# Kernel tuning notes

Hardware: AMD Instinct MI355X
Metric: run time of the kernel (lower is better)

Reference implementation:

```python
import jax, jax.numpy as jnp
import numpy as np

T, OBS, MLP, H, ACT = 2048, 512, 1024, 1024, 16
SIG0 = 0.5  # config['noise_std'] -> NoisyLinear init_std


def mish(x):
    return x * jnp.tanh(jax.nn.softplus(x))


def noisy_linear(x, wm, ws, bm, bs, kw, kb):
    # NoisyLinear: perturbed weights/bias sampled per forward call from the key.
    # In the original, the same key is tiled across the vmapped time axis, so a
    # single noise sample is shared by all timesteps -> one sample here.
    w = wm + ws * jax.random.normal(kw, wm.shape, wm.dtype)
    b = bm + bs * jax.random.normal(kb, bm.shape, bm.dtype)
    return x @ w.T + b


def setup_inputs() -> dict:
    key = jax.random.key(0)
    ks = jax.random.split(key, 8)

    def lin(k, o, i):
        lim = 1.0 / np.sqrt(i)
        return jax.random.uniform(k, (o, i), jnp.float32, -lim, lim)

    return {
        "x": jax.random.normal(ks[0], (T, OBS), jnp.float32),
        "state": jnp.zeros((H,), jnp.float32),
        "start": jax.random.randint(ks[1], (T,), 0, 2, dtype=jnp.int32),
        "done": jnp.zeros((T,), jnp.int32),
        "pre_wm": lin(ks[2], MLP, OBS),
        "pre_ws": jnp.full((MLP, OBS), SIG0, jnp.float32),
        "pre_bm": jnp.zeros((MLP,), jnp.float32),
        "pre_bs": jnp.full((MLP,), SIG0, jnp.float32),
        "gru_wih": lin(ks[3], 3 * H, MLP),
        "gru_whh": lin(ks[4], 3 * H, H),
        "gru_b": jnp.zeros((3 * H,), jnp.float32),
        "gru_bn": jnp.zeros((H,), jnp.float32),
        "p1_wm": lin(ks[5], MLP, H),
        "p1_ws": jnp.full((MLP, H), SIG0, jnp.float32),
        "p1_bm": jnp.zeros((MLP,), jnp.float32),
        "p1_bs": jnp.full((MLP,), SIG0, jnp.float32),
        "p2_wm": lin(ks[6], MLP, MLP),
        "p2_ws": jnp.full((MLP, MLP), SIG0, jnp.float32),
        "p2_bm": jnp.zeros((MLP,), jnp.float32),
        "p2_bs": jnp.full((MLP,), SIG0, jnp.float32),
        "p3_wm": lin(ks[7], ACT, MLP) * 0.01,  # final_layer_init: small last layer
        "p3_ws": jnp.full((ACT, MLP), SIG0, jnp.float32),
        "p3_bm": jnp.zeros((ACT,), jnp.float32),
        "p3_bs": jnp.full((ACT,), SIG0, jnp.float32),
    }


def _forward(x, state, start, pre_wm, pre_ws, pre_bm, pre_bs, gru_wih, gru_whh,
             gru_b, gru_bn, p1_wm, p1_ws, p1_bm, p1_bs, p2_wm, p2_ws, p2_bm,
             p2_bs, p3_wm, p3_ws, p3_bm, p3_bs):
    nk = jax.random.split(jax.random.key(7), 8)
    # pre MLP: NoisyLinear + mish, vectorized over time
    z = mish(noisy_linear(x, pre_wm, pre_ws, pre_bm, pre_bs, nk[0], nk[1]))  # [T, MLP]
    # input-side GRU gates precomputed as one big GEMM (equinox GRUCell math)
    igates = z @ gru_wih.T + gru_b  # [T, 3H]
    keep = (1 - start).astype(z.dtype)  # [T]; 0 where an episode starts -> reset h

    def step(h, inp):
        ig, k = inp
        h_in = h * k  # state * logical_not(start)
        hg = h_in @ gru_whh.T  # [3H]
        ir, iz, in_ = jnp.split(ig, 3)
        hr, hz, hn = jnp.split(hg, 3)
        r = jax.nn.sigmoid(ir + hr)
        u = jax.nn.sigmoid(iz + hz)
        n = jnp.tanh(in_ + r * (hn + gru_bn))
        h_new = n + u * (h_in - n)  # == (1-u)*n + u*h_in
        return h_new, h_new

    final_state, states = jax.lax.scan(step, state, (igates, keep))  # states: [T, H]
    # post MLP: NoisyLinear+mish, NoisyLinear+mish, NoisyLinear (final)
    y = mish(noisy_linear(states, p1_wm, p1_ws, p1_bm, p1_bs, nk[2], nk[3]))
    y = mish(noisy_linear(y, p2_wm, p2_ws, p2_bm, p2_bs, nk[4], nk[5]))
    y = noisy_linear(y, p3_wm, p3_ws, p3_bm, p3_bs, nk[6], nk[7])  # [T, ACT]
    return y, final_state


def reference(x, state, start, done, pre_wm, pre_ws, pre_bm, pre_bs, gru_wih,
              gru_whh, gru_b, gru_bn, p1_wm, p1_ws, p1_bm, p1_bs, p2_wm, p2_ws,
              p2_bm, p2_bs, p3_wm, p3_ws, p3_bm, p3_bs):
    del done  # threaded through the scan in the original but never used
    return _forward(x, state, start, pre_wm, pre_ws, pre_bm, pre_bs, gru_wih,
                    gru_whh, gru_b, gru_bn, p1_wm, p1_ws, p1_bm, p1_bs, p2_wm,
                    p2_ws, p2_bm, p2_bs, p3_wm, p3_ws, p3_bm, p3_bs)
```

## Files before the change

kernel.cpp:

```cpp
#include <hip/hip_runtime.h>
#include <cstdint>
#include <cstddef>

#define T_ 2048
#define OBS_ 512
#define MLP_ 1024
#define H_ 1024
#define ACT_ 16
#define H3_ 3072
#define NROUNDS 20

typedef short bf16x8 __attribute__((ext_vector_type(8)));
typedef float f32x4 __attribute__((ext_vector_type(4)));

__host__ __device__ __forceinline__ uint32_t rotl32(uint32_t v, int d) {
  return (v << d) | (v >> (32 - d));
}
__host__ __device__ __forceinline__ void tf2x32(uint32_t k0, uint32_t k1,
                                                uint32_t x0, uint32_t x1,
                                                uint32_t& o0, uint32_t& o1) {
  uint32_t ks2 = k0 ^ k1 ^ 0x1BD11BDAu;
  x0 += k0; x1 += k1;
  x0 += x1; x1 = rotl32(x1, 13); x1 ^= x0;
  x0 += x1; x1 = rotl32(x1, 15); x1 ^= x0;
  x0 += x1; x1 = rotl32(x1, 26); x1 ^= x0;
  x0 += x1; x1 = rotl32(x1, 6);  x1 ^= x0;
  x0 += k1; x1 += ks2 + 1u;
  x0 += x1; x1 = rotl32(x1, 17); x1 ^= x0;
  x0 += x1; x1 = rotl32(x1, 29); x1 ^= x0;
  x0 += x1; x1 = rotl32(x1, 16); x1 ^= x0;
  x0 += x1; x1 = rotl32(x1, 24); x1 ^= x0;
  x0 += ks2; x1 += k0 + 2u;
  x0 += x1; x1 = rotl32(x1, 13); x1 ^= x0;
  x0 += x1; x1 = rotl32(x1, 15); x1 ^= x0;
  x0 += x1; x1 = rotl32(x1, 26); x1 ^= x0;
  x0 += x1; x1 = rotl32(x1, 6);  x1 ^= x0;
  x0 += k0; x1 += k1 + 3u;
  x0 += x1; x1 = rotl32(x1, 17); x1 ^= x0;
  x0 += x1; x1 = rotl32(x1, 29); x1 ^= x0;
  x0 += x1; x1 = rotl32(x1, 16); x1 ^= x0;
  x0 += x1; x1 = rotl32(x1, 24); x1 ^= x0;
  x0 += k1; x1 += ks2 + 4u;
  x0 += x1; x1 = rotl32(x1, 13); x1 ^= x0;
  x0 += x1; x1 = rotl32(x1, 15); x1 ^= x0;
  x0 += x1; x1 = rotl32(x1, 26); x1 ^= x0;
  x0 += x1; x1 = rotl32(x1, 6);  x1 ^= x0;
  x0 += ks2; x1 += k0 + 5u;
  o0 = x0; o1 = x1;
}

__device__ __forceinline__ float erfinv_f32(float x) {
  float w = -log1pf(-x * x);
  float p;
  if (w < 5.0f) {
    w = w - 2.5f;
    p = 2.81022636e-08f;
    p = fmaf(p, w, 3.43273939e-07f);
    p = fmaf(p, w, -3.5233877e-06f);
    p = fmaf(p, w, -4.39150654e-06f);
    p = fmaf(p, w, 0.00021858087f);
    p = fmaf(p, w, -0.00125372503f);
    p = fmaf(p, w, -0.00417768164f);
    p = fmaf(p, w, 0.246640727f);
    p = fmaf(p, w, 1.50140941f);
  } else {
    w = sqrtf(w) - 3.0f;
    p = -0.000200214257f;
    p = fmaf(p, w, 0.000100950558f);
    p = fmaf(p, w, 0.00134934322f);
    p = fmaf(p, w, -0.00367342844f);
    p = fmaf(p, w, 0.00573950773f);
    p = fmaf(p, w, -0.0076224613f);
    p = fmaf(p, w, 0.00943887047f);
    p = fmaf(p, w, 1.00167406f);
    p = fmaf(p, w, 2.83297682f);
  }
  return p * x;
}

__device__ __forceinline__ float bits_to_normal(uint32_t bits) {
  const float lo = -0.99999994f;
  float f = __uint_as_float((bits >> 9) | 0x3f800000u) - 1.0f;
  float u = fmaf(f, 2.0f, lo);
  u = fmaxf(lo, u);
  return 1.41421356237f * erfinv_f32(u);
}

__device__ __forceinline__ float sigmoidf_(float x) {
  return 1.0f / (1.0f + expf(-x));
}
__device__ __forceinline__ float mishf_(float x) {
  float sp = fmaxf(x, 0.0f) + log1pf(expf(-fabsf(x)));
  return x * tanhf(sp);
}

__device__ __forceinline__ ushort f2bf(float v) {
  uint32_t u = __float_as_uint(v);
  uint32_t r = (u + 0x7FFFu + ((u >> 16) & 1u)) >> 16;
  return (ushort)r;
}
__device__ __forceinline__ float bf2f(ushort b) {
  return __uint_as_float(((uint32_t)b) << 16);
}

struct NoiseDesc {
  const float* wm; const float* ws;
  ushort* dh; ushort* dl; float* df;
  uint32_t k0, k1, base, mode;
};
struct NoiseArgs { NoiseDesc d[8]; uint32_t total; int* meta_zero; };

__global__ __launch_bounds__(256) void k_gen_noise(NoiseArgs a) {
  if (blockIdx.x < 16) a.meta_zero[blockIdx.x * 256 + threadIdx.x] = 0;
  uint32_t idx = blockIdx.x * 256u + threadIdx.x;
  for (; idx < a.total; idx += gridDim.x * 256u) {
    int ti = 0;
#pragma unroll
    for (int i = 1; i < 8; ++i) if (idx >= a.d[i].base) ti = i;
    NoiseDesc dd = a.d[ti];
    uint32_t j = idx - dd.base;
    uint32_t b1, b2;
    tf2x32(dd.k0, dd.k1, 0u, j, b1, b2);
    float v = fmaf(dd.ws[j], bits_to_normal(b1 ^ b2), dd.wm[j]);
    if (dd.mode) {
      ushort hb = f2bf(v);
      dd.dh[j] = hb;
      dd.dl[j] = f2bf(v - bf2f(hb));
    } else {
      dd.df[j] = v;
    }
  }
}

__global__ __launch_bounds__(256) void k_split(const float* __restrict__ in,
                                               ushort* __restrict__ h,
                                               ushort* __restrict__ l, int n4) {
  int i = blockIdx.x * 256 + threadIdx.x;
  if (i >= n4) return;
  float4 v = ((const float4*)in)[i];
  ushort4 hb, lb;
  hb.x = f2bf(v.x); lb.x = f2bf(v.x - bf2f(hb.x));
  hb.y = f2bf(v.y); lb.y = f2bf(v.y - bf2f(hb.y));
  hb.z = f2bf(v.z); lb.z = f2bf(v.z - bf2f(hb.z));
  hb.w = f2bf(v.w); lb.w = f2bf(v.w - bf2f(hb.w));
  ((ushort4*)h)[i] = hb;
  ((ushort4*)l)[i] = lb;
}

template <int ACTF, int OUTM>
__global__ __launch_bounds__(256, 2) void k_mgemm(
    const ushort* __restrict__ Ah, const ushort* __restrict__ Al,
    const ushort* __restrict__ Wh, const ushort* __restrict__ Wl,
    const float* __restrict__ bias,
    float* __restrict__ Cf, ushort* __restrict__ Ch, ushort* __restrict__ Cl,
    int K, int Nreal, int ldc) {
  __shared__ ushort sA[2][128 * 32];
  __shared__ ushort sW[2][128 * 32];
  const int tid = threadIdx.x;
  const int m0 = blockIdx.y * 128, n0 = blockIdx.x * 128;
  const int wid = tid >> 6, lane = tid & 63;
  const int wm = (wid >> 1) * 64, wn = (wid & 1) * 64;
  const int lr = lane & 15, lk = lane >> 4;
  const int r0 = tid >> 2;
  const int c0 = (tid & 3) * 8;
  f32x4 acc[4][4] = {};
  for (int k0 = 0; k0 < K; k0 += 32) {
    const size_t aoff0 = (size_t)(m0 + r0) * K + k0 + c0;
    const size_t aoff1 = (size_t)(m0 + r0 + 64) * K + k0 + c0;
    const size_t woff0 = (size_t)(n0 + r0) * K + k0 + c0;
    const size_t woff1 = (size_t)(n0 + r0 + 64) * K + k0 + c0;
    int4 ah0 = *(const int4*)(Ah + aoff0);
    int4 ah1 = *(const int4*)(Ah + aoff1);
    int4 al0 = *(const int4*)(Al + aoff0);
    int4 al1 = *(const int4*)(Al + aoff1);
    int4 wh0 = *(const int4*)(Wh + woff0);
    int4 wh1 = *(const int4*)(Wh + woff1);
    int4 wl0 = *(const int4*)(Wl + woff0);
    int4 wl1 = *(const int4*)(Wl + woff1);
    __syncthreads();
    *(int4*)(&sA[0][r0 * 32 + c0]) = ah0;
    *(int4*)(&sA[0][(r0 + 64) * 32 + c0]) = ah1;
    *(int4*)(&sA[1][r0 * 32 + c0]) = al0;
    *(int4*)(&sA[1][(r0 + 64) * 32 + c0]) = al1;
    *(int4*)(&sW[0][r0 * 32 + c0]) = wh0;
    *(int4*)(&sW[0][(r0 + 64) * 32 + c0]) = wh1;
    *(int4*)(&sW[1][r0 * 32 + c0]) = wl0;
    *(int4*)(&sW[1][(r0 + 64) * 32 + c0]) = wl1;
    __syncthreads();
    bf16x8 fah[4], fal[4], fwh[4], fwl[4];
#pragma unroll
    for (int f = 0; f < 4; ++f) {
      int ar = (wm + f * 16 + lr) * 32 + lk * 8;
      fah[f] = *(const bf16x8*)(&sA[0][ar]);
      fal[f] = *(const bf16x8*)(&sA[1][ar]);
      int wr = (wn + f * 16 + lr) * 32 + lk * 8;
      fwh[f] = *(const bf16x8*)(&sW[0][wr]);
      fwl[f] = *(const bf16x8*)(&sW[1][wr]);
    }
#pragma unroll
    for (int mf = 0; mf < 4; ++mf)
#pragma unroll
      for (int nf = 0; nf < 4; ++nf) {
        acc[mf][nf] = __builtin_amdgcn_mfma_f32_16x16x32_bf16(fah[mf], fwh[nf], acc[mf][nf], 0, 0, 0);
        acc[mf][nf] = __builtin_amdgcn_mfma_f32_16x16x32_bf16(fah[mf], fwl[nf], acc[mf][nf], 0, 0, 0);
        acc[mf][nf] = __builtin_amdgcn_mfma_f32_16x16x32_bf16(fal[mf], fwh[nf], acc[mf][nf], 0, 0, 0);
      }
  }
#pragma unroll
  for (int mf = 0; mf < 4; ++mf)
#pragma unroll
    for (int nf = 0; nf < 4; ++nf) {
      int col = n0 + wn + nf * 16 + lr;
      if (col >= Nreal) continue;
      float bv = bias[col];
#pragma unroll
      for (int r = 0; r < 4; ++r) {
        int row = m0 + wm + mf * 16 + lk * 4 + r;
        float v = acc[mf][nf][r] + bv;
        if (ACTF) v = mishf_(v);
        if (OUTM == 0) {
          Cf[(size_t)row * ldc + col] = v;
        } else {
          ushort hb = f2bf(v);
          Ch[(size_t)row * ldc + col] = hb;
          Cl[(size_t)row * ldc + col] = f2bf(v - bf2f(hb));
        }
      }
    }
}

__global__ void k_li(const int* __restrict__ start, int* __restrict__ li,
                     int* __restrict__ counts) {
  int t = blockIdx.x * 256 + threadIdx.x;
  if (t >= T_) return;
  int l = 0, tt = t;
  while (tt > 0 && start[tt] == 0) { tt--; l++; }
  li[t] = l;
  if (t > 0) atomicAdd(&counts[l], 1);
}

__global__ __launch_bounds__(256) void k_offsets(const int* __restrict__ counts,
                                                 int* __restrict__ offsets) {
  __shared__ int a[2048], b[2048];
  int tid = threadIdx.x;
  for (int i = tid; i < 2048; i += 256) a[i] = counts[i];
  __syncthreads();
  int* cur = a; int* nxt = b;
  for (int d = 1; d < 2048; d <<= 1) {
    for (int i = tid; i < 2048; i += 256)
      nxt[i] = cur[i] + (i >= d ? cur[i - d] : 0);
    __syncthreads();
    int* t_ = cur; cur = nxt; nxt = t_;
  }
  for (int i = tid; i < 2048; i += 256)
    offsets[i] = (i == 0) ? 0 : cur[i - 1];
}

__global__ void k_scatter(const int* __restrict__ li, const int* __restrict__ offsets,
                          int* __restrict__ cursors, int* __restrict__ list) {
  int t = blockIdx.x * 256 + threadIdx.x;
  if (t <= 0 || t >= T_) return;
  int l = li[t];
  int pos = atomicAdd(&cursors[l], 1);
  list[offsets[l] + pos] = t;
}

__global__ __launch_bounds__(256) void k_hg0(
    const float* __restrict__ whhf, const float* __restrict__ state0,
    const int* __restrict__ start, float* __restrict__ hg0) {
  const float keep0 = 1.0f - (float)start[0];
  int gw = blockIdx.x * 4 + (threadIdx.x >> 6);
  int lane = threadIdx.x & 63;
  for (int r = gw * 3; r < gw * 3 + 3 && r < H3_; ++r) {
    const float* wr = whhf + (size_t)r * H_;
    float s = 0.f;
    for (int c = lane; c < H_; c += 64) s = fmaf(wr[c], state0[c] * keep0, s);
    for (int o = 32; o; o >>= 1) s += __shfl_down(s, o, 64);
    if (lane == 0) hg0[r] = s;
  }
}

__global__ __launch_bounds__(256) void k_gate0(
    const float* __restrict__ ig, const float* __restrict__ gbn,
    const float* __restrict__ state0, const int* __restrict__ start,
    const int* __restrict__ counts, const int* __restrict__ offsets,
    const int* __restrict__ list, const float* __restrict__ hg0,
    ushort* __restrict__ st_h, ushort* __restrict__ st_l) {
  const float keep0 = 1.0f - (float)start[0];
  int cnt0 = counts[0], off0 = offsets[0];
  int total = (cnt0 + 1) * H_;
  for (int e = blockIdx.x * 256 + threadIdx.x; e < total; e += gridDim.x * 256) {
    int s = e >> 10, i = e & (H_ - 1);
    int t; float hin, hr, hz, hn;
    if (s == 0) {
      t = 0; hin = state0[i] * keep0;
      hr = hg0[i]; hz = hg0[H_ + i]; hn = hg0[2 * H_ + i];
    } else {
      t = list[off0 + s - 1]; hin = 0.f; hr = 0.f; hz = 0.f; hn = 0.f;
    }
    float ir = ig[(size_t)t * H3_ + i];
    float iz = ig[(size_t)t * H3_ + H_ + i];
    float in_ = ig[(size_t)t * H3_ + 2 * H_ + i];
    float r = sigmoidf_(ir + hr), u = sigmoidf_(iz + hz);
    float n = tanhf(in_ + r * (hn + gbn[i]));
    float v = n + u * (hin - n);
    ushort hb = f2bf(v);
    st_h[(size_t)t * H_ + i] = hb;
    st_l[(size_t)t * H_ + i] = f2bf(v - bf2f(hb));
  }
}

struct SMemRound {
  ushort Hs[2][64][40];
  ushort Bs[2][96][40];
  int tl[64];
};

__global__ __launch_bounds__(256) void k_round(
    const int k, const float* __restrict__ ig,
    const ushort* __restrict__ whh_h, const ushort* __restrict__ whh_l,
    const float* __restrict__ gbn,
    const int* __restrict__ counts, const int* __restrict__ offsets,
    const int* __restrict__ list,
    ushort* __restrict__ st_h, ushort* __restrict__ st_l) {
  const int cnt = counts[k];
  if (cnt == 0) return;
  __shared__ SMemRound sm;
  const int tid = threadIdx.x, bid = blockIdx.x, nb = gridDim.x;
  const int off = offsets[k];
  const int mtiles = (cnt + 63) >> 6;
  const int tiles = mtiles << 5;

  const int wid = tid >> 6, lane = tid & 63;
  const int lr = lane & 15, lk = lane >> 4;
  const int wm = (wid >> 1) * 32;
  const int wi = wid & 1;

  const int a_koct = tid & 3, a_row = (tid >> 2) & 63;
  int blev[3], brow[3], bkoct[3];
#pragma unroll
  for (int j = 0; j < 3; ++j) {
    int c = tid + 256 * j;
    blev[j] = c / 384;
    int rem = c - blev[j] * 384;
    brow[j] = rem >> 2;
    bkoct[j] = rem & 3;
  }
  const ushort* bsp[3];
#pragma unroll
  for (int j = 0; j < 3; ++j) bsp[j] = blev[j] ? whh_l : whh_h;

  for (int tile = bid; tile < tiles; tile += nb) {
    int mt = tile >> 5;
    int i0 = (tile & 31) << 5;
    __syncthreads();
    if (tid < 64) {
      int s = mt * 64 + tid;
      sm.tl[tid] = (s < cnt) ? list[off + s] : 0;
    }
    __syncthreads();

    size_t bsrc[3];
#pragma unroll
    for (int j = 0; j < 3; ++j)
      bsrc[j] = (size_t)((brow[j] >> 5) * H_ + i0 + (brow[j] & 31)) * H_ + bkoct[j] * 8;

    f32x4 acc[2][3] = {};
    int4 paA[2], paB[2], pbA[3], pbB[3];

#define LOADA(K0, DST)                                                        \
    {                                                                         \
      int t0_ = sm.tl[a_row];                                                 \
      DST[0] = make_int4(0, 0, 0, 0); DST[1] = make_int4(0, 0, 0, 0);         \
      if (t0_ > 0) {                                                          \
        size_t base_ = (size_t)(t0_ - 1) * H_ + (K0) + a_koct * 8;            \
        DST[0] = *(const int4*)(st_h + base_);                                \
        DST[1] = *(const int4*)(st_l + base_);                                \
      }                                                                       \
    }
#define LOADB(K0, DST)                                                        \
    {                                                                         \
      _Pragma("unroll")                                                       \
      for (int j = 0; j < 3; ++j)                                             \
        DST[j] = *(const int4*)(bsp[j] + bsrc[j] + (K0));                     \
    }
#define WRITEAB(PA, PB)                                                       \
    {                                                                         \
      *(int4*)(&sm.Hs[0][a_row][a_koct * 8]) = PA[0];                         \
      *(int4*)(&sm.Hs[1][a_row][a_koct * 8]) = PA[1];                         \
      _Pragma("unroll")                                                       \
      for (int j = 0; j < 3; ++j)                                             \
        *(int4*)(&sm.Bs[blev[j]][brow[j]][bkoct[j] * 8]) = PB[j];             \
    }
#define COMPUTE()                                                             \
    {                                                                         \
      bf16x8 ah[2], al[2], bh[3], bl[3];                                      \
      _Pragma("unroll")                                                       \
      for (int mf = 0; mf < 2; ++mf) {                                        \
        int row = wm + mf * 16 + lr;                                          \
        ah[mf] = *(const bf16x8*)(&sm.Hs[0][row][lk * 8]);                    \
        al[mf] = *(const bf16x8*)(&sm.Hs[1][row][lk * 8]);                    \
      }                                                                       \
      _Pragma("unroll")                                                       \
      for (int g = 0; g < 3; ++g) {                                           \
        int row = g * 32 + wi * 16 + lr;                                      \
        bh[g] = *(const bf16x8*)(&sm.Bs[0][row][lk * 8]);                     \
        bl[g] = *(const bf16x8*)(&sm.Bs[1][row][lk * 8]);                     \
      }                                                                       \
      _Pragma("unroll")                                                       \
      for (int mf = 0; mf < 2; ++mf)                                          \
        _Pragma("unroll")                                                     \
        for (int g = 0; g < 3; ++g) {                                         \
          acc[mf][g] = __builtin_amdgcn_mfma_f32_16x16x32_bf16(ah[mf], bh[g], acc[mf][g], 0, 0, 0); \
          acc[mf][g] = __builtin_amdgcn_mfma_f32_16x16x32_bf16(ah[mf], bl[g], acc[mf][g], 0, 0, 0); \
          acc[mf][g] = __builtin_amdgcn_mfma_f32_16x16x32_bf16(al[mf], bh[g], acc[mf][g], 0, 0, 0); \
        }                                                                     \
    }

    LOADA(0, paA); LOADB(0, pbA);
    LOADA(32, paB); LOADB(32, pbB);
    for (int k0 = 0; k0 < H_; k0 += 64) {
      __syncthreads();
      WRITEAB(paA, pbA);
      if (k0 + 64 < H_) { LOADA(k0 + 64, paA); LOADB(k0 + 64, pbA); }
      __syncthreads();
      COMPUTE();
      __syncthreads();
      WRITEAB(paB, pbB);
      if (k0 + 96 < H_) { LOADA(k0 + 96, paB); LOADB(k0 + 96, pbB); }
      __syncthreads();
      COMPUTE();
    }
#undef LOADA
#undef LOADB
#undef WRITEAB
#undef COMPUTE
    int i = i0 + wi * 16 + lr;
#pragma unroll
    for (int mf = 0; mf < 2; ++mf)
#pragma unroll
      for (int r = 0; r < 4; ++r) {
        int slot = wm + mf * 16 + lk * 4 + r;
        int t = sm.tl[slot];
        if (t <= 0) continue;
        size_t pidx = (size_t)(t - 1) * H_ + i;
        float hin = bf2f(st_h[pidx]) + bf2f(st_l[pidx]);
        float ir = ig[(size_t)t * H3_ + i];
        float iz = ig[(size_t)t * H3_ + H_ + i];
        float in_ = ig[(size_t)t * H3_ + 2 * H_ + i];
        float rr = sigmoidf_(ir + acc[mf][0][r]);
        float uu = sigmoidf_(iz + acc[mf][1][r]);
        float nn = tanhf(in_ + rr * (acc[mf][2][r] + gbn[i]));
        float v = nn + uu * (hin - nn);
        ushort hb = f2bf(v);
        st_h[(size_t)t * H_ + i] = hb;
        st_l[(size_t)t * H_ + i] = f2bf(v - bf2f(hb));
      }
  }
}

__global__ __launch_bounds__(256) void k_cleanup(
    const float* __restrict__ ig, const float* __restrict__ whhf,
    const float* __restrict__ gbn, const int* __restrict__ counts,
    const int* __restrict__ offsets, const int* __restrict__ list,
    ushort* __restrict__ st_h, ushort* __restrict__ st_l) {
  __shared__ float hbuf[H_];
  __shared__ float hg[H3_];
  const int tid = threadIdx.x;
  for (int k = NROUNDS; k < 2048; ++k) {
    int cnt = counts[k];
    if (cnt == 0) return;
    int off = offsets[k];
    for (int s = 0; s < cnt; ++s) {
      int t = list[off + s];
      for (int i = tid; i < H_; i += 256) {
        size_t p = (size_t)(t - 1) * H_ + i;
        hbuf[i] = bf2f(st_h[p]) + bf2f(st_l[p]);
      }
      __syncthreads();
      int wv = tid >> 6, ln = tid & 63;
      for (int r = wv; r < H3_; r += 4) {
        const float* wr = whhf + (size_t)r * H_;
        float sum = 0.f;
#pragma unroll 4
        for (int u = 0; u < 16; ++u) {
          int c = ln * 16 + u;
          sum = fmaf(wr[c], hbuf[c], sum);
        }
#pragma unroll
        for (int d = 32; d > 0; d >>= 1) sum += __shfl_down(sum, d, 64);
        if (ln == 0) hg[r] = sum;
      }
      __syncthreads();
      for (int i = tid; i < H_; i += 256) {
        float hin = hbuf[i];
        float r_ = sigmoidf_(ig[(size_t)t * H3_ + i] + hg[i]);
        float u_ = sigmoidf_(ig[(size_t)t * H3_ + H_ + i] + hg[H_ + i]);
        float n_ = tanhf(ig[(size_t)t * H3_ + 2 * H_ + i] + r_ * (hg[2 * H_ + i] + gbn[i]));
        float v = n_ + u_ * (hin - n_);
        ushort hb = f2bf(v);
        st_h[(size_t)t * H_ + i] = hb;
        st_l[(size_t)t * H_ + i] = f2bf(v - bf2f(hb));
      }
      __syncthreads();
    }
  }
}

__global__ void k_final(const ushort* __restrict__ st_h,
                        const ushort* __restrict__ st_l,
                        float* __restrict__ out) {
  int i = blockIdx.x * 256 + threadIdx.x;
  if (i < H_)
    out[T_ * ACT_ + i] = bf2f(st_h[(size_t)(T_ - 1) * H_ + i]) +
                         bf2f(st_l[(size_t)(T_ - 1) * H_ + i]);
}

extern "C" void kernel_launch(void* const* d_in, const int* in_sizes, int n_in,
                              void* d_out, int out_size, void* d_ws, size_t ws_size,
                              hipStream_t stream) {
  const float* x      = (const float*)d_in[0];
  const float* state0 = (const float*)d_in[1];
  const int*   start  = (const int*)d_in[2];
  const float* pre_wm = (const float*)d_in[4];
  const float* pre_ws = (const float*)d_in[5];
  const float* pre_bm = (const float*)d_in[6];
  const float* pre_bs = (const float*)d_in[7];
  const float* gru_wih = (const float*)d_in[8];
  const float* gru_whh = (const float*)d_in[9];
  const float* gru_b  = (const float*)d_in[10];
  const float* gru_bn = (const float*)d_in[11];
  const float* p1_wm = (const float*)d_in[12];
  const float* p1_ws = (const float*)d_in[13];
  const float* p1_bm = (const float*)d_in[14];
  const float* p1_bs = (const float*)d_in[15];
  const float* p2_wm = (const float*)d_in[16];
  const float* p2_ws = (const float*)d_in[17];
  const float* p2_bm = (const float*)d_in[18];
  const float* p2_bs = (const float*)d_in[19];
  const float* p3_wm = (const float*)d_in[20];
  const float* p3_ws = (const float*)d_in[21];
  const float* p3_bm = (const float*)d_in[22];
  const float* p3_bs = (const float*)d_in[23];

  char* p = (char*)d_ws;
  auto nxt = [&](size_t bytes) { char* r = p; p += (bytes + 255) & ~255ul; return r; };
  ushort* wihh = (ushort*)nxt((size_t)H3_ * MLP_ * 2);
  ushort* wihl = (ushort*)nxt((size_t)H3_ * MLP_ * 2);
  ushort* preWh = (ushort*)nxt((size_t)MLP_ * OBS_ * 2);
  ushort* preWl = (ushort*)nxt((size_t)MLP_ * OBS_ * 2);
  ushort* p1Wh = (ushort*)nxt((size_t)MLP_ * H_ * 2);
  ushort* p1Wl = (ushort*)nxt((size_t)MLP_ * H_ * 2);
  ushort* p2Wh = (ushort*)nxt((size_t)MLP_ * MLP_ * 2);
  ushort* p2Wl = (ushort*)nxt((size_t)MLP_ * MLP_ * 2);
  ushort* p3Wh = (ushort*)nxt((size_t)128 * MLP_ * 2);
  ushort* p3Wl = (ushort*)nxt((size_t)128 * MLP_ * 2);
  float* preB = (float*)nxt(MLP_ * 4);
  float* p1B  = (float*)nxt(MLP_ * 4);
  float* p2B  = (float*)nxt(MLP_ * 4);
  float* p3B  = (float*)nxt(ACT_ * 4);
  ushort* B1h = (ushort*)nxt((size_t)T_ * MLP_ * 2);
  ushort* B1l = (ushort*)nxt((size_t)T_ * MLP_ * 2);
  ushort* B2h = (ushort*)nxt((size_t)T_ * MLP_ * 2);
  ushort* B2l = (ushort*)nxt((size_t)T_ * MLP_ * 2);
  float* igb = (float*)nxt((size_t)T_ * H3_ * 4);
  float* hg0 = (float*)nxt(H3_ * 4);
  int* counts  = (int*)nxt(2048 * 4);
  int* cursors = (int*)nxt(2048 * 4);
  int* li      = (int*)nxt(2048 * 4);
  int* offsets = (int*)nxt(2048 * 4);
  int* list    = (int*)nxt(2048 * 4);

  uint32_t nk0[8], nk1[8];
  for (int i = 0; i < 8; ++i) {
    uint32_t b1, b2;
    tf2x32(0u, 7u, 0u, (uint32_t)i, b1, b2);
    nk0[i] = b1; nk1[i] = b2;
  }

  NoiseArgs na;
  const float* wms[8] = {pre_wm, pre_bm, p1_wm, p1_bm, p2_wm, p2_bm, p3_wm, p3_bm};
  const float* wss[8] = {pre_ws, pre_bs, p1_ws, p1_bs, p2_ws, p2_bs, p3_ws, p3_bs};
  ushort* dhs[8] = {preWh, nullptr, p1Wh, nullptr, p2Wh, nullptr, p3Wh, nullptr};
  ushort* dls[8] = {preWl, nullptr, p1Wl, nullptr, p2Wl, nullptr, p3Wl, nullptr};
  float* dfs[8]  = {nullptr, preB, nullptr, p1B, nullptr, p2B, nullptr, p3B};
  uint32_t ns[8] = {MLP_ * OBS_, MLP_, MLP_ * H_, MLP_, MLP_ * MLP_, MLP_, ACT_ * MLP_, ACT_};
  uint32_t base = 0;
  for (int i = 0; i < 8; ++i) {
    na.d[i].wm = wms[i]; na.d[i].ws = wss[i];
    na.d[i].dh = dhs[i]; na.d[i].dl = dls[i]; na.d[i].df = dfs[i];
    na.d[i].k0 = nk0[i]; na.d[i].k1 = nk1[i];
    na.d[i].base = base; na.d[i].mode = (i & 1) ? 0u : 1u;
    base += ns[i];
  }
  na.total = base;
  na.meta_zero = counts;

  dim3 b256(256);

  hipMemsetAsync(p3Wh + 16 * MLP_, 0, (size_t)112 * MLP_ * 2, stream);
  hipMemsetAsync(p3Wl + 16 * MLP_, 0, (size_t)112 * MLP_ * 2, stream);

  k_gen_noise<<<dim3(4096), b256, 0, stream>>>(na);
  k_split<<<dim3((H3_ * MLP_ / 4) / 256), b256, 0, stream>>>(gru_wih, wihh, wihl, H3_ * MLP_ / 4);
  k_split<<<dim3((T_ * OBS_ / 4) / 256), b256, 0, stream>>>(x, B2h, B2l, T_ * OBS_ / 4);

  k_li<<<dim3(T_ / 256), b256, 0, stream>>>(start, li, counts);
  k_offsets<<<dim3(1), b256, 0, stream>>>(counts, offsets);
  k_scatter<<<dim3(T_ / 256), b256, 0, stream>>>(li, offsets, cursors, list);
  k_hg0<<<dim3(256), b256, 0, stream>>>(gru_whh, state0, start, hg0);

  k_mgemm<1, 1><<<dim3(MLP_ / 128, T_ / 128), b256, 0, stream>>>(
      B2h, B2l, preWh, preWl, preB, nullptr, B1h, B1l, OBS_, MLP_, MLP_);
  k_mgemm<0, 0><<<dim3(H3_ / 128, T_ / 128), b256, 0, stream>>>(
      B1h, B1l, wihh, wihl, gru_b, igb, nullptr, nullptr, MLP_, H3_, H3_);

  k_split<<<dim3((H3_ * H_ / 4) / 256), b256, 0, stream>>>(gru_whh, wihh, wihl, H3_ * H_ / 4);

  k_gate0<<<dim3(512), b256, 0, stream>>>(igb, gru_bn, state0, start, counts,
                                          offsets, list, hg0, B2h, B2l);
  for (int k = 1; k < NROUNDS; ++k)
    k_round<<<dim3(512), b256, 0, stream>>>(k, igb, wihh, wihl, gru_bn, counts,
                                            offsets, list, B2h, B2l);
  k_cleanup<<<dim3(1), b256, 0, stream>>>(igb, gru_whh, gru_bn, counts, offsets,
                                          list, B2h, B2l);

  k_final<<<dim3(4), b256, 0, stream>>>(B2h, B2l, (float*)d_out);

  k_mgemm<1, 1><<<dim3(MLP_ / 128, T_ / 128), b256, 0, stream>>>(
      B2h, B2l, p1Wh, p1Wl, p1B, nullptr, B1h, B1l, H_, MLP_, MLP_);
  k_mgemm<1, 1><<<dim3(MLP_ / 128, T_ / 128), b256, 0, stream>>>(
      B1h, B1l, p2Wh, p2Wl, p2B, nullptr, B2h, B2l, MLP_, MLP_, MLP_);
  k_mgemm<0, 0><<<dim3(1, T_ / 128), b256, 0, stream>>>(
      B2h, B2l, p3Wh, p3Wl, p3B, (float*)d_out, nullptr, nullptr, MLP_, ACT_, ACT_);
}
```

Before: 996.0 us.

## Shrink GEMM N-tile to 64 and prefetch global tiles two steps ahead

```diff
diff --git a/kernel.cpp b/kernel.cpp
--- a/kernel.cpp
+++ b/kernel.cpp
@@ -155,61 +155,86 @@
     float* __restrict__ Cf, ushort* __restrict__ Ch, ushort* __restrict__ Cl,
     int K, int Nreal, int ldc) {
   __shared__ ushort sA[2][128 * 32];
-  __shared__ ushort sW[2][128 * 32];
+  __shared__ ushort sW[2][64 * 32];
   const int tid = threadIdx.x;
-  const int m0 = blockIdx.y * 128, n0 = blockIdx.x * 128;
+  const int m0 = blockIdx.y * 128, n0 = blockIdx.x * 64;
   const int wid = tid >> 6, lane = tid & 63;
-  const int wm = (wid >> 1) * 64, wn = (wid & 1) * 64;
+  const int wm = (wid >> 1) * 64, wn = (wid & 1) * 32;
   const int lr = lane & 15, lk = lane >> 4;
   const int r0 = tid >> 2;
   const int c0 = (tid & 3) * 8;
-  f32x4 acc[4][4] = {};
-  for (int k0 = 0; k0 < K; k0 += 32) {
-    const size_t aoff0 = (size_t)(m0 + r0) * K + k0 + c0;
-    const size_t aoff1 = (size_t)(m0 + r0 + 64) * K + k0 + c0;
-    const size_t woff0 = (size_t)(n0 + r0) * K + k0 + c0;
-    const size_t woff1 = (size_t)(n0 + r0 + 64) * K + k0 + c0;
-    int4 ah0 = *(const int4*)(Ah + aoff0);
-    int4 ah1 = *(const int4*)(Ah + aoff1);
-    int4 al0 = *(const int4*)(Al + aoff0);
-    int4 al1 = *(const int4*)(Al + aoff1);
-    int4 wh0 = *(const int4*)(Wh + woff0);
-    int4 wh1 = *(const int4*)(Wh + woff1);
-    int4 wl0 = *(const int4*)(Wl + woff0);
-    int4 wl1 = *(const int4*)(Wl + woff1);
+  f32x4 acc[4][2] = {};
+
+  int4 paA[4], pwA[2], paB[4], pwB[2];
+
+#define LOADAB(K0, PA, PW)                                                    \
+  {                                                                           \
+    size_t a0_ = (size_t)(m0 + r0) * K + (K0) + c0;                           \
+    size_t a1_ = (size_t)(m0 + r0 + 64) * K + (K0) + c0;                      \
+    PA[0] = *(const int4*)(Ah + a0_);                                         \
+    PA[1] = *(const int4*)(Ah + a1_);                                         \
+    PA[2] = *(const int4*)(Al + a0_);                                         \
+    PA[3] = *(const int4*)(Al + a1_);                                         \
+    size_t w0_ = (size_t)(n0 + r0) * K + (K0) + c0;                           \
+    PW[0] = *(const int4*)(Wh + w0_);                                         \
+    PW[1] = *(const int4*)(Wl + w0_);                                         \
+  }
+#define WRITEAB(PA, PW)                                                       \
+  {                                                                           \
+    *(int4*)(&sA[0][r0 * 32 + c0]) = PA[0];                                   \
+    *(int4*)(&sA[0][(r0 + 64) * 32 + c0]) = PA[1];                            \
+    *(int4*)(&sA[1][r0 * 32 + c0]) = PA[2];                                   \
+    *(int4*)(&sA[1][(r0 + 64) * 32 + c0]) = PA[3];                            \
+    *(int4*)(&sW[0][r0 * 32 + c0]) = PW[0];                                   \
+    *(int4*)(&sW[1][r0 * 32 + c0]) = PW[1];                                   \
+  }
+#define COMPUTE()                                                             \
+  {                                                                           \
+    bf16x8 fah[4], fal[4], fwh[2], fwl[2];                                    \
+    _Pragma("unroll")                                                         \
+    for (int mf = 0; mf < 4; ++mf) {                                          \
+      int ar = (wm + mf * 16 + lr) * 32 + lk * 8;                             \
+      fah[mf] = *(const bf16x8*)(&sA[0][ar]);                                 \
+      fal[mf] = *(const bf16x8*)(&sA[1][ar]);                                 \
+    }                                                                         \
+    _Pragma("unroll")                                                         \
+    for (int nf = 0; nf < 2; ++nf) {                                          \
+      int wr = (wn + nf * 16 + lr) * 32 + lk * 8;                             \
+      fwh[nf] = *(const bf16x8*)(&sW[0][wr]);                                 \
+      fwl[nf] = *(const bf16x8*)(&sW[1][wr]);                                 \
+    }                                                                         \
+    _Pragma("unroll")                                                         \
+    for (int mf = 0; mf < 4; ++mf)                                            \
+      _Pragma("unroll")                                                       \
+      for (int nf = 0; nf < 2; ++nf) {                                        \
+        acc[mf][nf] = __builtin_amdgcn_mfma_f32_16x16x32_bf16(fah[mf], fwh[nf], acc[mf][nf], 0, 0, 0); \
+        acc[mf][nf] = __builtin_amdgcn_mfma_f32_16x16x32_bf16(fah[mf], fwl[nf], acc[mf][nf], 0, 0, 0); \
+        acc[mf][nf] = __builtin_amdgcn_mfma_f32_16x16x32_bf16(fal[mf], fwh[nf], acc[mf][nf], 0, 0, 0); \
+      }                                                                       \
+  }
+
+  LOADAB(0, paA, pwA);
+  LOADAB(32, paB, pwB);
+  for (int k0 = 0; k0 < K; k0 += 64) {
     __syncthreads();
-    *(int4*)(&sA[0][r0 * 32 + c0]) = ah0;
-    *(int4*)(&sA[0][(r0 + 64) * 32 + c0]) = ah1;
-    *(int4*)(&sA[1][r0 * 32 + c0]) = al0;
-    *(int4*)(&sA[1][(r0 + 64) * 32 + c0]) = al1;
-    *(int4*)(&sW[0][r0 * 32 + c0]) = wh0;
-    *(int4*)(&sW[0][(r0 + 64) * 32 + c0]) = wh1;
-    *(int4*)(&sW[1][r0 * 32 + c0]) = wl0;
-    *(int4*)(&sW[1][(r0 + 64) * 32 + c0]) = wl1;
+    WRITEAB(paA, pwA);
+    if (k0 + 64 < K) LOADAB(k0 + 64, paA, pwA);
     __syncthreads();
-    bf16x8 fah[4], fal[4], fwh[4], fwl[4];
-#pragma unroll
-    for (int f = 0; f < 4; ++f) {
-      int ar = (wm + f * 16 + lr) * 32 + lk * 8;
-      fah[f] = *(const bf16x8*)(&sA[0][ar]);
-      fal[f] = *(const bf16x8*)(&sA[1][ar]);
-      int wr = (wn + f * 16 + lr) * 32 + lk * 8;
-      fwh[f] = *(const bf16x8*)(&sW[0][wr]);
-      fwl[f] = *(const bf16x8*)(&sW[1][wr]);
-    }
-#pragma unroll
-    for (int mf = 0; mf < 4; ++mf)
-#pragma unroll
-      for (int nf = 0; nf < 4; ++nf) {
-        acc[mf][nf] = __builtin_amdgcn_mfma_f32_16x16x32_bf16(fah[mf], fwh[nf], acc[mf][nf], 0, 0, 0);
-        acc[mf][nf] = __builtin_amdgcn_mfma_f32_16x16x32_bf16(fah[mf], fwl[nf], acc[mf][nf], 0, 0, 0);
-        acc[mf][nf] = __builtin_amdgcn_mfma_f32_16x16x32_bf16(fal[mf], fwh[nf], acc[mf][nf], 0, 0, 0);
-      }
-  }
+    COMPUTE();
+    __syncthreads();
+    WRITEAB(paB, pwB);
+    if (k0 + 96 < K) LOADAB(k0 + 96, paB, pwB);
+    __syncthreads();
+    COMPUTE();
+  }
+#undef LOADAB
+#undef WRITEAB
+#undef COMPUTE
+
 #pragma unroll
   for (int mf = 0; mf < 4; ++mf)
 #pragma unroll
-    for (int nf = 0; nf < 4; ++nf) {
+    for (int nf = 0; nf < 2; ++nf) {
       int col = n0 + wn + nf * 16 + lr;
       if (col >= Nreal) continue;
       float bv = bias[col];
@@ -598,8 +623,8 @@
 
   dim3 b256(256);
 
-  hipMemsetAsync(p3Wh + 16 * MLP_, 0, (size_t)112 * MLP_ * 2, stream);
-  hipMemsetAsync(p3Wl + 16 * MLP_, 0, (size_t)112 * MLP_ * 2, stream);
+  hipMemsetAsync(p3Wh + 16 * MLP_, 0, (size_t)48 * MLP_ * 2, stream);
+  hipMemsetAsync(p3Wl + 16 * MLP_, 0, (size_t)48 * MLP_ * 2, stream);
 
   k_gen_noise<<<dim3(4096), b256, 0, stream>>>(na);
   k_split<<<dim3((H3_ * MLP_ / 4) / 256), b256, 0, stream>>>(gru_wih, wihh, wihl, H3_ * MLP_ / 4);
@@ -610,9 +635,9 @@
   k_scatter<<<dim3(T_ / 256), b256, 0, stream>>>(li, offsets, cursors, list);
   k_hg0<<<dim3(256), b256, 0, stream>>>(gru_whh, state0, start, hg0);
 
-  k_mgemm<1, 1><<<dim3(MLP_ / 128, T_ / 128), b256, 0, stream>>>(
+  k_mgemm<1, 1><<<dim3(MLP_ / 64, T_ / 128), b256, 0, stream>>>(
       B2h, B2l, preWh, preWl, preB, nullptr, B1h, B1l, OBS_, MLP_, MLP_);
-  k_mgemm<0, 0><<<dim3(H3_ / 128, T_ / 128), b256, 0, stream>>>(
+  k_mgemm<0, 0><<<dim3(H3_ / 64, T_ / 128), b256, 0, stream>>>(
       B1h, B1l, wihh, wihl, gru_b, igb, nullptr, nullptr, MLP_, H3_, H3_);
 
   k_split<<<dim3((H3_ * H_ / 4) / 256), b256, 0, stream>>>(gru_whh, wihh, wihl, H3_ * H_ / 4);
@@ -627,9 +652,9 @@
 
   k_final<<<dim3(4), b256, 0, stream>>>(B2h, B2l, (float*)d_out);
 
-  k_mgemm<1, 1><<<dim3(MLP_ / 128, T_ / 128), b256, 0, stream>>>(
+  k_mgemm<1, 1><<<dim3(MLP_ / 64, T_ / 128), b256, 0, stream>>>(
       B2h, B2l, p1Wh, p1Wl, p1B, nullptr, B1h, B1l, H_, MLP_, MLP_);
-  k_mgemm<1, 1><<<dim3(MLP_ / 128, T_ / 128), b256, 0, stream>>>(
+  k_mgemm<1, 1><<<dim3(MLP_ / 64, T_ / 128), b256, 0, stream>>>(
       B1h, B1l, p2Wh, p2Wl, p2B, nullptr, B2h, B2l, MLP_, MLP_, MLP_);
   k_mgemm<0, 0><<<dim3(1, T_ / 128), b256, 0, stream>>>(
       B2h, B2l, p3Wh, p3Wl, p3B, (float*)d_out, nullptr, nullptr, MLP_, ACT_, ACT_);
```

Measured after the change: 1.225 ms. +23.0%, slower.
